# Kernel tuning notes

Measured on AMD Instinct MI355X. Metric: run time of the kernel, lower is better.

The kernel has to match this reference:

```python
import jax, jax.numpy as jnp
import numpy as np

NEG_SLOPE = 0.2
NUM_NODES = 100000
NUM_EDGES = 200000
NNZ = 1600000
IN_C = 128
OUT_C = 128
STAR = 64


def setup_inputs() -> dict:
    key = jax.random.key(0)
    ks = jax.random.split(key, 12)
    X = jax.random.normal(ks[0], (NUM_NODES, IN_C), dtype=jnp.float32)
    V = jax.random.randint(ks[1], (NNZ,), 0, NUM_NODES)
    E = jax.random.randint(ks[2], (NNZ,), 0, NUM_EDGES)
    S_features = jax.random.normal(ks[3], (NUM_EDGES, STAR), dtype=jnp.float32)
    s = 1.0 / np.sqrt(IN_C)
    Wx = jax.random.uniform(ks[4], (IN_C, OUT_C), minval=-s, maxval=s)
    bx = jax.random.uniform(ks[5], (OUT_C,), minval=-s, maxval=s)
    Wv = jax.random.uniform(ks[6], (IN_C, OUT_C), minval=-s, maxval=s)
    bv = jax.random.uniform(ks[7], (OUT_C,), minval=-s, maxval=s)
    sa = 1.0 / np.sqrt(OUT_C)
    a_vec = jax.random.uniform(ks[8], (OUT_C,), minval=-sa, maxval=sa)
    st = 1.0 / np.sqrt(OUT_C + STAR)
    Wt = jax.random.uniform(ks[9], (OUT_C + STAR, OUT_C), minval=-st, maxval=st)
    bt = jax.random.uniform(ks[10], (OUT_C,), minval=-st, maxval=st)
    return {"X": X, "V": V, "E": E, "S_features": S_features,
            "Wx": Wx, "bx": bx, "Wv": Wv, "bv": bv,
            "a_vec": a_vec, "Wt": Wt, "bt": bt}


def _segment_softmax(s, seg, num_segments):
    m = jax.ops.segment_max(s, seg, num_segments=num_segments)
    e = jnp.exp(s - m[seg])
    denom = jax.ops.segment_sum(e, seg, num_segments=num_segments)
    return e / denom[seg]


def reference(X, V, E, S_features, Wx, bx, Wv, bv, a_vec, Wt, bt):
    # DPHGNNConv forward (eval mode: dropout = identity)
    X_init = X @ Wx + bx                      # [N, out]
    X_feat = X @ Wv + bv                      # [N, out]
    scores = X_feat @ a_vec                   # [N]
    s = jax.nn.leaky_relu(scores[V], NEG_SLOPE)  # [nnz]
    w = _segment_softmax(s, E, NUM_EDGES)     # [nnz]
    Xev = X_feat[V] * w[:, None]              # [nnz, out]
    Y_v2e = jax.ops.segment_sum(Xev, E, num_segments=NUM_EDGES)
    Y_v2e = jax.nn.elu(Y_v2e)
    e_msg = jnp.concatenate([Y_v2e, S_features], axis=1)  # [E, out+star]
    Y = e_msg @ Wt + bt                       # [E, out]
    Yev = Y[E]                                # [nnz, out]
    num = jax.ops.segment_sum(Yev, V, num_segments=NUM_NODES)
    cnt = jax.ops.segment_sum(jnp.ones((NNZ,), jnp.float32), V, num_segments=NUM_NODES)
    Xn = num / jnp.maximum(cnt, 1.0)[:, None]  # scatter_mean
    Xn = jax.nn.elu(Xn)                        # is_last=False
    return Xn + X_init
```

## Files before the change

### kernel.cpp

```cpp
#include <hip/hip_runtime.h>
#include <math.h>

#define N_NODES 100000
#define N_EDGES 200000
#define NNZ_    1600000
#define INC  128
#define OUTC 128
#define STAR_ 64
#define NEG 0.2f
#define NBIN_E 391
#define NBIN_V 196
#define NBIN (NBIN_E + NBIN_V)
#define CHUNK 4000
#define NBLK_A (NNZ_/CHUNK)
#define CAP_E 5120
#define CAP_V 9216
#define PAIR_SZ (NBIN_E*CAP_E + NBIN_V*CAP_V)
#define CAPI 288
#define CAPN 288

typedef __attribute__((ext_vector_type(8))) short bf16x8_t;
typedef __attribute__((ext_vector_type(8))) unsigned short u16x8;
typedef __attribute__((ext_vector_type(4))) float f32x4_t;

__device__ __forceinline__ float leaky(float x){ return x > 0.f ? x : NEG*x; }
__device__ __forceinline__ float elu1(float x){ return x > 0.f ? x : __expf(x)-1.f; }
__device__ __forceinline__ unsigned short f2bf(float f){
  unsigned u = __float_as_uint(f);
  unsigned r = u + 0x7FFFu + ((u >> 16) & 1u);
  return (unsigned short)(r >> 16);
}
__device__ __forceinline__ float bf2f(unsigned short h){
  return __uint_as_float(((unsigned)h) << 16);
}
__device__ __forceinline__ int padBaseD(int bin){
  return bin < NBIN_E ? bin*CAP_E : NBIN_E*CAP_E + (bin-NBIN_E)*CAP_V;
}

__global__ void k_cvt(const float* __restrict__ Wx, const float* __restrict__ Wv,
                      const float* __restrict__ Wt,
                      unsigned short* __restrict__ WcatT, unsigned short* __restrict__ WtT,
                      int* __restrict__ binCur){
  const int i = blockIdx.x*256 + threadIdx.x;
  if (i < 256*128){
    const int n = i >> 7, k = i & 127;
    const float v = (n < 128) ? Wx[k*128 + n] : Wv[k*128 + (n-128)];
    WcatT[n*128 + k] = f2bf(v);
  }
  const int j = i - 256*128;
  if (j >= 0 && j < 128*192){
    const int n = j / 192, k = j - n*192;
    WtT[n*192 + k] = f2bf(Wt[k*128 + n]);
  }
  if (blockIdx.x == 0){
    for (int p = threadIdx.x; p < NBIN; p += 256) binCur[p] = padBaseD(p);
  }
}

__global__ __launch_bounds__(256) void k_front(
    const float* __restrict__ X, const unsigned short* __restrict__ WcatT,
    const float* __restrict__ bx, const float* __restrict__ bv,
    const float* __restrict__ av,
    float* __restrict__ Xinit, unsigned short* __restrict__ Xfb,
    float* __restrict__ scores,
    const int* __restrict__ V, const int* __restrict__ E,
    int* __restrict__ binCur, int2* __restrict__ pair){
  __shared__ int hA[NBIN];
  __shared__ int baseA[NBIN];
  __shared__ unsigned short xb[16][136];
  __shared__ float sc[16];
  const int tid = threadIdx.x;

  if (blockIdx.x < NBLK_A) {
    for (int p = tid; p < NBIN; p += 256) hA[p] = 0;
    __syncthreads();
    const int start = blockIdx.x*CHUNK, end = start + CHUNK;
    for (int i = start + tid; i < end; i += 256){
      atomicAdd(&hA[E[i] >> 9], 1);
      atomicAdd(&hA[NBIN_E + (V[i] >> 9)], 1);
    }
    __syncthreads();
    for (int p = tid; p < NBIN; p += 256)
      baseA[p] = hA[p] ? atomicAdd(&binCur[p], hA[p]) : 0;
    __syncthreads();
    for (int p = tid; p < NBIN; p += 256) hA[p] = 0;
    __syncthreads();
    for (int i = start + tid; i < end; i += 256){
      const int e = E[i], v = V[i];
      const int be = e >> 9, bv_ = NBIN_E + (v >> 9);
      const int se = baseA[be]  + atomicAdd(&hA[be],  1);
      const int sv = baseA[bv_] + atomicAdd(&hA[bv_], 1);
      pair[se] = make_int2(e, v);
      pair[sv] = make_int2(v, e);
    }
    return;
  }

  const int lane = tid & 63, w = tid >> 6;
  const int quad = lane >> 4, l16 = lane & 15;
  const int r0 = (blockIdx.x - NBLK_A) * 16;
  if (tid < 16) sc[tid] = 0.f;
  {
    const int r = tid >> 4;
    const int c0 = (tid & 15) * 8;
    const float4 a4 = *(const float4*)&X[(size_t)(r0+r)*INC + c0];
    const float4 b4 = *(const float4*)&X[(size_t)(r0+r)*INC + c0 + 4];
    bf16x8_t pk;
    pk[0]=(short)f2bf(a4.x); pk[1]=(short)f2bf(a4.y); pk[2]=(short)f2bf(a4.z); pk[3]=(short)f2bf(a4.w);
    pk[4]=(short)f2bf(b4.x); pk[5]=(short)f2bf(b4.y); pk[6]=(short)f2bf(b4.z); pk[7]=(short)f2bf(b4.w);
    *(bf16x8_t*)&xb[r][c0] = pk;
  }
  __syncthreads();
  f32x4_t acc[4] = {{0,0,0,0},{0,0,0,0},{0,0,0,0},{0,0,0,0}};
  const int n_base = w*64 + l16;
  for (int s = 0; s < 4; ++s){
    const bf16x8_t af = *(const bf16x8_t*)&xb[l16][s*32 + quad*8];
    #pragma unroll
    for (int nt = 0; nt < 4; ++nt){
      const int n = n_base + nt*16;
      const bf16x8_t bf = *(const bf16x8_t*)&WcatT[(size_t)n*128 + s*32 + quad*8];
      acc[nt] = __builtin_amdgcn_mfma_f32_16x16x32_bf16(af, bf, acc[nt], 0, 0, 0);
    }
  }
  float pr[4] = {0.f, 0.f, 0.f, 0.f};
  #pragma unroll
  for (int nt = 0; nt < 4; ++nt){
    const int n = n_base + nt*16;
    const float bias = (n < 128) ? bx[n] : bv[n-128];
    #pragma unroll
    for (int r = 0; r < 4; ++r){
      const int m = quad*4 + r;
      const float val = acc[nt][r] + bias;
      if (n < 128) Xinit[(size_t)(r0+m)*OUTC + n] = val;
      else {
        Xfb[(size_t)(r0+m)*OUTC + (n-128)] = f2bf(val);
        pr[r] += val * av[n-128];
      }
    }
  }
  if (w >= 2){
    #pragma unroll
    for (int r = 0; r < 4; ++r) atomicAdd(&sc[quad*4 + r], pr[r]);
  }
  __syncthreads();
  if (tid < 16) scores[r0 + tid] = sc[tid];
}

__global__ __launch_bounds__(1024) void k_binscan(const int* __restrict__ binCur,
                                                  int* __restrict__ binBase, int* __restrict__ binCnt,
                                                  int2* __restrict__ vw, int* __restrict__ eIdxV){
  __shared__ int s[1024];
  const int tid = threadIdx.x;
  const int v = (tid < NBIN) ? (binCur[tid] - padBaseD(tid)) : 0;
  s[tid] = v; __syncthreads();
  for (int o = 1; o < 1024; o <<= 1){
    const int u = (tid >= o) ? s[tid-o] : 0;
    __syncthreads();
    s[tid] += u;
    __syncthreads();
  }
  if (tid < NBIN){ binBase[tid] = s[tid] - v; binCnt[tid] = v; }
  if (tid < 16){ vw[NNZ_ + tid] = make_int2(0, 0); eIdxV[NNZ_ + tid] = 0; }
}

__global__ __launch_bounds__(512) void k_binB(const int2* __restrict__ pair,
    const int* __restrict__ binBase, const int* __restrict__ binCnt,
    const float* __restrict__ scores,
    int2* __restrict__ vw, int* __restrict__ eIdxV,
    int* __restrict__ cntE, int* __restrict__ startsE,
    int* __restrict__ cntV, int* __restrict__ startsV,
    float* __restrict__ dens){
  __shared__ int h[512], sc0[512], sc1[512];
  __shared__ float dsh[512];
  const int bin = blockIdx.x;
  const bool isE = bin < NBIN_E;
  const int nb = isE ? bin : bin - NBIN_E;
  const int bucket0 = nb << 9;
  const int nBuckTot = isE ? N_EDGES : N_NODES;
  const int pstart = padBaseD(bin);
  const int n = binCnt[bin];
  const int itemBase = isE ? binBase[bin] : binBase[bin] - NNZ_;
  const int tid = threadIdx.x;
  h[tid] = 0; dsh[tid] = 0.f;
  __syncthreads();
  for (int j = tid; j < n; j += 512) atomicAdd(&h[pair[pstart + j].x & 511], 1);
  __syncthreads();
  sc0[tid] = h[tid];
  __syncthreads();
  int* a = sc0; int* b = sc1;
  for (int o = 1; o < 512; o <<= 1){
    b[tid] = a[tid] + (tid >= o ? a[tid-o] : 0);
    __syncthreads();
    int* t = a; a = b; b = t;
  }
  {
    const int excl = a[tid] - h[tid];
    b[tid] = itemBase + excl;
    const int bucket = bucket0 + tid;
    if (bucket < nBuckTot){
      if (isE){ cntE[bucket] = h[tid]; startsE[bucket] = itemBase + excl; }
      else    { cntV[bucket] = h[tid]; startsV[bucket] = itemBase + excl; }
    }
  }
  __syncthreads();
  for (int j = tid; j < n; j += 512){
    const int2 kv = pair[pstart + j];
    const int slot = atomicAdd(&b[kv.x & 511], 1);
    if (isE){
      const float ex = __expf(leaky(scores[kv.y]));
      vw[slot] = make_int2(kv.y, __float_as_int(ex));
      atomicAdd(&dsh[kv.x & 511], ex);
    } else {
      eIdxV[slot] = kv.y;
    }
  }
  __syncthreads();
  if (isE){
    const int bucket = bucket0 + tid;
    if (bucket < N_EDGES) dens[bucket] = dsh[tid];
  }
}

__global__ __launch_bounds__(256) void k_edge(
    const int* __restrict__ cntE, const int* __restrict__ startsE,
    const int2* __restrict__ vw, const float* __restrict__ dens,
    const unsigned short* __restrict__ Xfb,
    const float* __restrict__ S, const unsigned short* __restrict__ WtT,
    const float* __restrict__ bt, unsigned short* __restrict__ Ybf) {
  __shared__ int2 inc[CAPI + 8];
  __shared__ unsigned short msg[16][200];
  const int tid = threadIdx.x;
  const int lane = tid & 63, w = tid >> 6;
  const int e0 = blockIdx.x * 16;
  const int g16 = tid >> 4, s16 = tid & 15;

  const int st0 = startsE[e0];
  const int lim = startsE[e0 + 15] + cntE[e0 + 15] - st0;

  for (int i = tid; i < CAPI + 8; i += 256)
    inc[i] = (i < lim) ? vw[st0 + i] : make_int2(0, 0);

  {
    const float4 s4 = *(const float4*)&S[(size_t)(e0+g16)*STAR_ + s16*4];
    ushort4 pk; pk.x=f2bf(s4.x); pk.y=f2bf(s4.y); pk.z=f2bf(s4.z); pk.w=f2bf(s4.w);
    *(ushort4*)&msg[g16][128 + s16*4] = pk;
  }
  __syncthreads();

  const int e = e0 + g16;
  const int deg = cntE[e];
  const int lo  = startsE[e] - st0;
  const int c8 = s16 * 8;
  float ac[8] = {0.f,0.f,0.f,0.f,0.f,0.f,0.f,0.f};
  if (lo + deg <= CAPI) {
    for (int j = 0; j < deg; j += 8) {
      int2 pp[8];
      #pragma unroll
      for (int k = 0; k < 8; ++k) pp[k] = inc[lo + j + k];
      u16x8 xx[8];
      #pragma unroll
      for (int k = 0; k < 8; ++k)
        xx[k] = *(const u16x8*)&Xfb[(size_t)pp[k].x*OUTC + c8];
      #pragma unroll
      for (int k = 0; k < 8; ++k) {
        const float wgt = (j + k < deg) ? __int_as_float(pp[k].y) : 0.f;
        #pragma unroll
        for (int q = 0; q < 8; ++q) ac[q] += wgt * bf2f(xx[k][q]);
      }
    }
  } else {
    const int st = st0 + lo;
    for (int j = 0; j < deg; j += 8) {
      int2 pp[8];
      #pragma unroll
      for (int k = 0; k < 8; ++k) pp[k] = vw[st + j + k];
      u16x8 xx[8];
      #pragma unroll
      for (int k = 0; k < 8; ++k)
        xx[k] = *(const u16x8*)&Xfb[(size_t)pp[k].x*OUTC + c8];
      #pragma unroll
      for (int k = 0; k < 8; ++k) {
        const float wgt = (j + k < deg) ? __int_as_float(pp[k].y) : 0.f;
        #pragma unroll
        for (int q = 0; q < 8; ++q) ac[q] += wgt * bf2f(xx[k][q]);
      }
    }
  }
  {
    const float invd = deg > 0 ? 1.f/dens[e] : 0.f;
    u16x8 pk;
    #pragma unroll
    for (int q = 0; q < 8; ++q) pk[q] = f2bf(elu1(ac[q]*invd));
    *(u16x8*)&msg[g16][c8] = pk;
  }
  __syncthreads();

  const int quad = lane >> 4, l16 = lane & 15;
  f32x4_t acc0 = {0,0,0,0}, acc1 = {0,0,0,0};
  const int n0 = w * 32;
  for (int s = 0; s < 6; ++s) {
    const bf16x8_t af = *(const bf16x8_t*)&msg[l16][s*32 + quad*8];
    const bf16x8_t b0 = *(const bf16x8_t*)&WtT[(size_t)(n0 + l16)*192      + s*32 + quad*8];
    const bf16x8_t b1 = *(const bf16x8_t*)&WtT[(size_t)(n0 + 16 + l16)*192 + s*32 + quad*8];
    acc0 = __builtin_amdgcn_mfma_f32_16x16x32_bf16(af, b0, acc0, 0, 0, 0);
    acc1 = __builtin_amdgcn_mfma_f32_16x16x32_bf16(af, b1, acc1, 0, 0, 0);
  }
  const float bt0 = bt[n0 + l16], bt1 = bt[n0 + 16 + l16];
  #pragma unroll
  for (int r = 0; r < 4; ++r) {
    const int m = quad*4 + r;
    Ybf[(size_t)(e0+m)*OUTC + n0 + l16]      = f2bf(acc0[r] + bt0);
    Ybf[(size_t)(e0+m)*OUTC + n0 + 16 + l16] = f2bf(acc1[r] + bt1);
  }
}

__global__ __launch_bounds__(256) void k_node(
    const int* __restrict__ cntV, const int* __restrict__ startsV,
    const int* __restrict__ eIdxV,
    const unsigned short* __restrict__ Ybf, float* __restrict__ out) {
  __shared__ int elds[CAPN + 8];
  const int tid = threadIdx.x;
  const int sub = tid & 31, grp = tid >> 5;
  const int v0 = blockIdx.x * 8;

  const int st0 = startsV[v0];
  const int lim = startsV[v0 + 7] + cntV[v0 + 7] - st0;
  for (int i = tid; i < CAPN + 8; i += 256)
    elds[i] = (i < lim) ? eIdxV[st0 + i] : 0;
  __syncthreads();

  const int v = v0 + grp;
  const int c4 = sub * 4;
  const int deg = cntV[v];
  const int lo  = startsV[v] - st0;
  float a0=0.f, a1=0.f, a2=0.f, a3=0.f;
  if (lo + deg <= CAPN) {
    for (int j = 0; j < deg; j += 8) {
      int ee[8];
      #pragma unroll
      for (int k = 0; k < 8; ++k) ee[k] = elds[lo + j + k];
      ushort4 yy[8];
      #pragma unroll
      for (int k = 0; k < 8; ++k)
        yy[k] = *(const ushort4*)&Ybf[(size_t)ee[k]*OUTC + c4];
      #pragma unroll
      for (int k = 0; k < 8; ++k) {
        const float pz = (j + k < deg) ? 1.f : 0.f;
        a0 += pz * bf2f(yy[k].x); a1 += pz * bf2f(yy[k].y);
        a2 += pz * bf2f(yy[k].z); a3 += pz * bf2f(yy[k].w);
      }
    }
  } else {
    const int st = st0 + lo;
    for (int j = 0; j < deg; j += 8) {
      int ee[8];
      #pragma unroll
      for (int k = 0; k < 8; ++k) ee[k] = eIdxV[st + j + k];
      ushort4 yy[8];
      #pragma unroll
      for (int k = 0; k < 8; ++k)
        yy[k] = *(const ushort4*)&Ybf[(size_t)ee[k]*OUTC + c4];
      #pragma unroll
      for (int k = 0; k < 8; ++k) {
        const float pz = (j + k < deg) ? 1.f : 0.f;
        a0 += pz * bf2f(yy[k].x); a1 += pz * bf2f(yy[k].y);
        a2 += pz * bf2f(yy[k].z); a3 += pz * bf2f(yy[k].w);
      }
    }
  }
  const float invd = 1.f / fmaxf((float)deg, 1.f);
  float4 o = *(float4*)&out[(size_t)v*OUTC + c4];
  o.x = elu1(a0*invd) + o.x;
  o.y = elu1(a1*invd) + o.y;
  o.z = elu1(a2*invd) + o.z;
  o.w = elu1(a3*invd) + o.w;
  *(float4*)&out[(size_t)v*OUTC + c4] = o;
}

extern "C" void kernel_launch(void* const* d_in, const int* in_sizes, int n_in,
                              void* d_out, int out_size, void* d_ws, size_t ws_size,
                              hipStream_t stream) {
  const float* X  = (const float*)d_in[0];
  const int*   V  = (const int*)d_in[1];
  const int*   E  = (const int*)d_in[2];
  const float* S  = (const float*)d_in[3];
  const float* Wx = (const float*)d_in[4];
  const float* bx = (const float*)d_in[5];
  const float* Wv = (const float*)d_in[6];
  const float* bv = (const float*)d_in[7];
  const float* av = (const float*)d_in[8];
  const float* Wt = (const float*)d_in[9];
  const float* bt = (const float*)d_in[10];
  float* out = (float*)d_out;

  char* ws = (char*)d_ws;
  size_t off = 0;
  auto alloc = [&](size_t bytes) -> void* {
    off = (off + 255) & ~(size_t)255;
    void* p = ws + off; off += bytes; return p;
  };
  unsigned short* Xfb   = (unsigned short*)alloc((size_t)N_NODES*OUTC*2);
  unsigned short* Ybf   = (unsigned short*)alloc((size_t)N_EDGES*OUTC*2);
  float* scores = (float*)alloc((size_t)N_NODES*4);
  unsigned short* WcatT = (unsigned short*)alloc((size_t)256*128*2);
  unsigned short* WtT   = (unsigned short*)alloc((size_t)128*192*2);
  int2* pair   = (int2*)alloc((size_t)PAIR_SZ*8);
  int* binBase = (int*)alloc((size_t)NBIN*4);
  int* binCur  = (int*)alloc((size_t)NBIN*4);
  int* binCnt  = (int*)alloc((size_t)NBIN*4);
  int* cntE    = (int*)alloc((size_t)N_EDGES*4);
  int* cntV    = (int*)alloc((size_t)N_NODES*4);
  int* startsE = (int*)alloc((size_t)N_EDGES*4);
  int* startsV = (int*)alloc((size_t)N_NODES*4);
  int2* vw     = (int2*)alloc((size_t)(NNZ_+16)*8);
  int* eIdxV   = (int*)alloc((size_t)(NNZ_+16)*4);
  float* dens  = (float*)alloc((size_t)N_EDGES*4);

  k_cvt<<<(256*128 + 128*192 + 255)/256, 256, 0, stream>>>(Wx, Wv, Wt, WcatT, WtT, binCur);
  k_front<<<NBLK_A + N_NODES/16, 256, 0, stream>>>(X, WcatT, bx, bv, av, out, Xfb, scores,
                                                   V, E, binCur, pair);
  k_binscan<<<1, 1024, 0, stream>>>(binCur, binBase, binCnt, vw, eIdxV);
  k_binB<<<NBIN, 512, 0, stream>>>(pair, binBase, binCnt, scores, vw, eIdxV,
                                   cntE, startsE, cntV, startsV, dens);

  k_edge<<<N_EDGES/16, 256, 0, stream>>>(cntE, startsE, vw, dens, Xfb, S, WtT, bt, Ybf);
  k_node<<<N_NODES/8, 256, 0, stream>>>(cntV, startsV, eIdxV, Ybf, out);
}
```

Measured before the change: 473.7 us.

## Drop bin-scan kernel and overlap node-bin sorting with edge compute

Removes the single-block k_binscan launch. Each binning block now computes its own base offset by reducing the counts of all earlier bins. The node-side bin sort is moved out of k_binB and merged as extra leading blocks into the edge kernel, so it can run alongside the edge aggregation and GEMM work. This saves one launch and a serial stage, at the cost of redundant prefix reductions in every block and a larger, more heterogeneous edge kernel.

```diff
diff --git a/kernel.cpp b/kernel.cpp
--- a/kernel.cpp
+++ b/kernel.cpp
@@ -40,7 +40,8 @@
 __global__ void k_cvt(const float* __restrict__ Wx, const float* __restrict__ Wv,
                       const float* __restrict__ Wt,
                       unsigned short* __restrict__ WcatT, unsigned short* __restrict__ WtT,
-                      int* __restrict__ binCur){
+                      int* __restrict__ binCur,
+                      int2* __restrict__ vw, int* __restrict__ eIdxV){
   const int i = blockIdx.x*256 + threadIdx.x;
   if (i < 256*128){
     const int n = i >> 7, k = i & 127;
@@ -54,6 +55,7 @@
   }
   if (blockIdx.x == 0){
     for (int p = threadIdx.x; p < NBIN; p += 256) binCur[p] = padBaseD(p);
+    if (threadIdx.x < 16){ vw[NNZ_ + threadIdx.x] = make_int2(0, 0); eIdxV[NNZ_ + threadIdx.x] = 0; }
   }
 }
 
@@ -146,41 +148,26 @@
   if (tid < 16) scores[r0 + tid] = sc[tid];
 }
 
-__global__ __launch_bounds__(1024) void k_binscan(const int* __restrict__ binCur,
-                                                  int* __restrict__ binBase, int* __restrict__ binCnt,
-                                                  int2* __restrict__ vw, int* __restrict__ eIdxV){
-  __shared__ int s[1024];
-  const int tid = threadIdx.x;
-  const int v = (tid < NBIN) ? (binCur[tid] - padBaseD(tid)) : 0;
-  s[tid] = v; __syncthreads();
-  for (int o = 1; o < 1024; o <<= 1){
-    const int u = (tid >= o) ? s[tid-o] : 0;
-    __syncthreads();
-    s[tid] += u;
-    __syncthreads();
-  }
-  if (tid < NBIN){ binBase[tid] = s[tid] - v; binCnt[tid] = v; }
-  if (tid < 16){ vw[NNZ_ + tid] = make_int2(0, 0); eIdxV[NNZ_ + tid] = 0; }
-}
-
-__global__ __launch_bounds__(512) void k_binB(const int2* __restrict__ pair,
-    const int* __restrict__ binBase, const int* __restrict__ binCnt,
-    const float* __restrict__ scores,
-    int2* __restrict__ vw, int* __restrict__ eIdxV,
-    int* __restrict__ cntE, int* __restrict__ startsE,
-    int* __restrict__ cntV, int* __restrict__ startsV,
+__global__ __launch_bounds__(512) void k_binBE(const int2* __restrict__ pair,
+    const int* __restrict__ binCur, const float* __restrict__ scores,
+    int2* __restrict__ vw, int* __restrict__ cntE, int* __restrict__ startsE,
     float* __restrict__ dens){
   __shared__ int h[512], sc0[512], sc1[512];
   __shared__ float dsh[512];
   const int bin = blockIdx.x;
-  const bool isE = bin < NBIN_E;
-  const int nb = isE ? bin : bin - NBIN_E;
-  const int bucket0 = nb << 9;
-  const int nBuckTot = isE ? N_EDGES : N_NODES;
+  const int bucket0 = bin << 9;
   const int pstart = padBaseD(bin);
-  const int n = binCnt[bin];
-  const int itemBase = isE ? binBase[bin] : binBase[bin] - NNZ_;
+  const int n = binCur[bin] - pstart;
   const int tid = threadIdx.x;
+  {
+    int part = 0;
+    for (int p = tid; p < bin; p += 512) part += binCur[p] - padBaseD(p);
+    sc0[tid] = part;
+    __syncthreads();
+    for (int o = 256; o; o >>= 1){ if (tid < o) sc0[tid] += sc0[tid+o]; __syncthreads(); }
+  }
+  const int itemBase = sc0[0];
+  __syncthreads();
   h[tid] = 0; dsh[tid] = 0.f;
   __syncthreads();
   for (int j = tid; j < n; j += 512) atomicAdd(&h[pair[pstart + j].x & 511], 1);
@@ -197,41 +184,80 @@
     const int excl = a[tid] - h[tid];
     b[tid] = itemBase + excl;
     const int bucket = bucket0 + tid;
-    if (bucket < nBuckTot){
-      if (isE){ cntE[bucket] = h[tid]; startsE[bucket] = itemBase + excl; }
-      else    { cntV[bucket] = h[tid]; startsV[bucket] = itemBase + excl; }
-    }
+    if (bucket < N_EDGES){ cntE[bucket] = h[tid]; startsE[bucket] = itemBase + excl; }
   }
   __syncthreads();
   for (int j = tid; j < n; j += 512){
     const int2 kv = pair[pstart + j];
     const int slot = atomicAdd(&b[kv.x & 511], 1);
-    if (isE){
-      const float ex = __expf(leaky(scores[kv.y]));
-      vw[slot] = make_int2(kv.y, __float_as_int(ex));
-      atomicAdd(&dsh[kv.x & 511], ex);
-    } else {
-      eIdxV[slot] = kv.y;
-    }
-  }
-  __syncthreads();
-  if (isE){
-    const int bucket = bucket0 + tid;
-    if (bucket < N_EDGES) dens[bucket] = dsh[tid];
-  }
-}
-
-__global__ __launch_bounds__(256) void k_edge(
+    const float ex = __expf(leaky(scores[kv.y]));
+    vw[slot] = make_int2(kv.y, __float_as_int(ex));
+    atomicAdd(&dsh[kv.x & 511], ex);
+  }
+  __syncthreads();
+  if (bucket0 + tid < N_EDGES) dens[bucket0 + tid] = dsh[tid];
+}
+
+__global__ __launch_bounds__(256) void k_edgeV(
     const int* __restrict__ cntE, const int* __restrict__ startsE,
     const int2* __restrict__ vw, const float* __restrict__ dens,
     const unsigned short* __restrict__ Xfb,
     const float* __restrict__ S, const unsigned short* __restrict__ WtT,
-    const float* __restrict__ bt, unsigned short* __restrict__ Ybf) {
-  __shared__ int2 inc[CAPI + 8];
-  __shared__ unsigned short msg[16][200];
+    const float* __restrict__ bt, unsigned short* __restrict__ Ybf,
+    const int2* __restrict__ pair, const int* __restrict__ binCur,
+    int* __restrict__ eIdxV, int* __restrict__ cntV, int* __restrict__ startsV) {
+  __shared__ __align__(16) char smem[(CAPI + 8)*8 + 16*200*2];
   const int tid = threadIdx.x;
+
+  if (blockIdx.x < NBIN_V) {
+    int* h   = (int*)smem;
+    int* sc0 = h + 512;
+    int* sc1 = sc0 + 512;
+    const int nb = blockIdx.x;
+    const int bin = NBIN_E + nb;
+    const int bucket0 = nb << 9;
+    const int pstart = padBaseD(bin);
+    const int n = binCur[bin] - pstart;
+    {
+      int part = 0;
+      for (int p = tid; p < bin; p += 256) part += binCur[p] - padBaseD(p);
+      sc0[tid] = part;
+      __syncthreads();
+      for (int o = 128; o; o >>= 1){ if (tid < o) sc0[tid] += sc0[tid+o]; __syncthreads(); }
+    }
+    const int itemBase = sc0[0] - NNZ_;
+    __syncthreads();
+    for (int p = tid; p < 512; p += 256) h[p] = 0;
+    __syncthreads();
+    for (int j = tid; j < n; j += 256) atomicAdd(&h[pair[pstart + j].x & 511], 1);
+    __syncthreads();
+    for (int p = tid; p < 512; p += 256) sc0[p] = h[p];
+    __syncthreads();
+    int* a = sc0; int* b = sc1;
+    for (int o = 1; o < 512; o <<= 1){
+      for (int p = tid; p < 512; p += 256) b[p] = a[p] + (p >= o ? a[p-o] : 0);
+      __syncthreads();
+      int* t = a; a = b; b = t;
+    }
+    for (int p = tid; p < 512; p += 256){
+      const int excl = a[p] - h[p];
+      b[p] = itemBase + excl;
+      const int bucket = bucket0 + p;
+      if (bucket < N_NODES){ cntV[bucket] = h[p]; startsV[bucket] = itemBase + excl; }
+    }
+    __syncthreads();
+    for (int j = tid; j < n; j += 256){
+      const int2 kv = pair[pstart + j];
+      const int slot = atomicAdd(&b[kv.x & 511], 1);
+      eIdxV[slot] = kv.y;
+    }
+    return;
+  }
+
+  int2* inc = (int2*)smem;
+  unsigned short (*msg)[200] = (unsigned short (*)[200])(smem + (CAPI + 8)*8);
   const int lane = tid & 63, w = tid >> 6;
-  const int e0 = blockIdx.x * 16;
+  const int e0 = (blockIdx.x - NBIN_V) * 16;
   const int g16 = tid >> 4, s16 = tid & 15;
 
   const int st0 = startsE[e0];
@@ -405,9 +431,7 @@
   unsigned short* WcatT = (unsigned short*)alloc((size_t)256*128*2);
   unsigned short* WtT   = (unsigned short*)alloc((size_t)128*192*2);
   int2* pair   = (int2*)alloc((size_t)PAIR_SZ*8);
-  int* binBase = (int*)alloc((size_t)NBIN*4);
   int* binCur  = (int*)alloc((size_t)NBIN*4);
-  int* binCnt  = (int*)alloc((size_t)NBIN*4);
   int* cntE    = (int*)alloc((size_t)N_EDGES*4);
   int* cntV    = (int*)alloc((size_t)N_NODES*4);
   int* startsE = (int*)alloc((size_t)N_EDGES*4);
@@ -416,13 +440,12 @@
   int* eIdxV   = (int*)alloc((size_t)(NNZ_+16)*4);
   float* dens  = (float*)alloc((size_t)N_EDGES*4);
 
-  k_cvt<<<(256*128 + 128*192 + 255)/256, 256, 0, stream>>>(Wx, Wv, Wt, WcatT, WtT, binCur);
+  k_cvt<<<(256*128 + 128*192 + 255)/256, 256, 0, stream>>>(Wx, Wv, Wt, WcatT, WtT,
+                                                           binCur, vw, eIdxV);
   k_front<<<NBLK_A + N_NODES/16, 256, 0, stream>>>(X, WcatT, bx, bv, av, out, Xfb, scores,
                                                    V, E, binCur, pair);
-  k_binscan<<<1, 1024, 0, stream>>>(binCur, binBase, binCnt, vw, eIdxV);
-  k_binB<<<NBIN, 512, 0, stream>>>(pair, binBase, binCnt, scores, vw, eIdxV,
-                                   cntE, startsE, cntV, startsV, dens);
-
-  k_edge<<<N_EDGES/16, 256, 0, stream>>>(cntE, startsE, vw, dens, Xfb, S, WtT, bt, Ybf);
+  k_binBE<<<NBIN_E, 512, 0, stream>>>(pair, binCur, scores, vw, cntE, startsE, dens);
+  k_edgeV<<<NBIN_V + N_EDGES/16, 256, 0, stream>>>(cntE, startsE, vw, dens, Xfb, S, WtT, bt, Ybf,
+                                                   pair, binCur, eIdxV, cntV, startsV);
   k_node<<<N_NODES/8, 256, 0, stream>>>(cntV, startsV, eIdxV, Ybf, out);
 }
```

After: 470.0 us. About the same (-0.8%).
